# Kernel tuning notes

Measured on AMD Instinct MI355X. Metric: run time of the kernel, lower is better.

Reference implementation:

```python
import jax, jax.numpy as jnp
import numpy as np

B, S, D = 2, 2048, 1024
H = 16
K = 21  # tisa_num_kernels
HD = D // H


def setup_inputs() -> dict:
    key = jax.random.key(0)
    ks = jax.random.split(key, 7)
    x = jax.random.normal(ks[0], (B, S, D), dtype=jnp.float32)
    # in_proj: Linear(d_model, 3*d_model, bias=False); stored as (D, 3D) for x @ w
    w_in = jax.random.normal(ks[1], (D, 3 * D), dtype=jnp.float32) * (1.0 / np.sqrt(D))
    # gate: Linear(d_model, 2*d_model) with bias
    w_gate = jax.random.normal(ks[2], (D, 2 * D), dtype=jnp.float32) * (1.0 / np.sqrt(D))
    b_gate = jnp.zeros((2 * D,), dtype=jnp.float32)
    # TISA kernel params, one set of K kernels per head
    amplitudes = jax.random.normal(ks[3], (H, K), dtype=jnp.float32) * 0.1
    sharpness = jax.random.uniform(ks[4], (H, K), dtype=jnp.float32, minval=0.05, maxval=0.3)
    max_fv, min_fv = S // 2, 5
    offsets = jax.random.uniform(ks[5], (H, K), dtype=jnp.float32, minval=-float(max_fv), maxval=float(max_fv))
    return {"x": x, "w_in": w_in, "w_gate": w_gate, "b_gate": b_gate,
            "amplitudes": amplitudes, "sharpness": sharpness, "offsets": offsets}


def _tisa_bias(amplitudes, sharpness, offsets, seq_len):
    # Translation-invariant: score depends only on relative position j - i.
    # Compute scores over the 2S-1 unique relative positions, then gather.
    rel = jnp.arange(-(seq_len - 1), seq_len, dtype=jnp.float32)  # (2S-1,)
    # (H, K, 2S-1)
    d = rel[None, None, :] - offsets[:, :, None]
    scores = amplitudes[:, :, None] * jnp.exp(-jnp.abs(sharpness)[:, :, None] * d * d)
    scores = scores.sum(axis=1)  # (H, 2S-1)
    idx = jnp.arange(seq_len)
    rel_idx = idx[None, :] - idx[:, None] + (seq_len - 1)  # (S, S) in [0, 2S-2]
    return scores[:, rel_idx]  # (H, S, S)


def reference(x, w_in, w_gate, b_gate, amplitudes, sharpness, offsets):
    b, s, d = x.shape
    proj = x @ w_in  # (B, S, 3D); layout: [k | v | q]
    k, v, q = jnp.split(proj, 3, axis=-1)

    def heads(t):  # (B, S, D) -> (B, H, S, HD)
        return t.reshape(b, s, H, HD).transpose(0, 2, 1, 3)

    q, k, v = heads(q), heads(k), heads(v)
    scale = 1.0 / jnp.sqrt(jnp.float32(HD))
    scores = jnp.einsum('bhqd,bhkd->bhqk', q, k) * scale  # (B, H, S, S)
    scores = scores + _tisa_bias(amplitudes, sharpness, offsets, s)[None]
    weights = jax.nn.softmax(scores, axis=-1)
    attn = jnp.einsum('bhqk,bhkd->bhqd', weights, v)  # (B, H, S, HD)
    out = attn.transpose(0, 2, 1, 3).reshape(b, s, d)  # (B, S, D)
    gated = out @ w_gate + b_gate  # (B, S, 2D)
    a, g = jnp.split(gated, 2, axis=-1)
    return a * jax.nn.sigmoid(g)
```

## Files before the change

### kernel.cpp

```cpp
#include <hip/hip_runtime.h>
#include <math.h>

#define B_   2
#define S_   2048
#define D_   1024
#define H_   16
#define K_   21
#define HD_  64
#define D3_  3072
#define D2_  2048
#define REL_ 4095
#define LOG2E 1.44269504f

typedef __attribute__((ext_vector_type(8))) short bf16x8;
typedef __attribute__((ext_vector_type(8))) unsigned short u16x8;
typedef __attribute__((ext_vector_type(4))) float f32x4;

#define MFMA16(a, b, c) __builtin_amdgcn_mfma_f32_16x16x32_bf16((a), (b), (c), 0, 0, 0)

__device__ __forceinline__ unsigned short f2bf(float f) {
    union { float f; unsigned u; } v; v.f = f;
    return (unsigned short)((v.u + 0x7fffu + ((v.u >> 16) & 1u)) >> 16);
}
__device__ __forceinline__ float bf2f(unsigned short h) {
    union { unsigned u; float f; } v; v.u = ((unsigned)h) << 16;
    return v.f;
}
__device__ __forceinline__ float asf(unsigned u) {
    union { unsigned u; float f; } v; v.u = u; return v.f;
}
__device__ __forceinline__ float fexp2(float x) {
    float r;
    asm("v_exp_f32 %0, %1" : "=v"(r) : "v"(x));
    return r;
}
__device__ __forceinline__ unsigned cvtpk(float a, float b) {
    unsigned r;
    asm("v_cvt_pk_bf16_f32 %0, %1, %2" : "=v"(r) : "v"(a), "v"(b));
    return r;
}
#define SPLIT8(f, ph, pl)                                                      \
    {                                                                          \
        _Pragma("unroll")                                                      \
        for (int _t = 0; _t < 4; ++_t) ph.u[_t] = cvtpk(f[2*_t], f[2*_t+1]);   \
        _Pragma("unroll")                                                      \
        for (int _t = 0; _t < 4; ++_t) {                                       \
            float _h0 = asf(ph.u[_t] << 16);                                   \
            float _h1 = asf(ph.u[_t] & 0xffff0000u);                           \
            pl.u[_t] = cvtpk(f[2*_t] - _h0, f[2*_t+1] - _h1);                  \
        }                                                                      \
    }

__device__ __forceinline__ void gload16(const void* g, void* l) {
    __builtin_amdgcn_global_load_lds(
        (const __attribute__((address_space(1))) unsigned int*)g,
        (__attribute__((address_space(3))) unsigned int*)l, 16, 0, 0);
}

__global__ void tisa_bias_kernel(const float* __restrict__ amp,
                                 const float* __restrict__ shp,
                                 const float* __restrict__ off,
                                 float* __restrict__ bias_rel) {
    int idx = blockIdx.x * blockDim.x + threadIdx.x;
    if (idx >= H_ * REL_) return;
    int h = idx / REL_;
    int r = idx - h * REL_;
    float rel = (float)(r - (S_ - 1));
    float acc = 0.f;
    #pragma unroll
    for (int k = 0; k < K_; ++k) {
        float d = rel - off[h * K_ + k];
        acc = fmaf(amp[h * K_ + k], expf(-fabsf(shp[h * K_ + k]) * d * d), acc);
    }
    bias_rel[idx] = acc * LOG2E;
}

__global__ __launch_bounds__(256) void convert_x_kernel(
    const float* __restrict__ in, unsigned short* __restrict__ out)
{
    const int t   = blockIdx.x * 256 + threadIdx.x;
    const int row = t >> 7;
    const int c8  = (t & 127) * 8;
    const float* src = in + (size_t)row * D_ + c8;
    float v[8];
    *(float4*)&v[0] = *(const float4*)src;
    *(float4*)&v[4] = *(const float4*)(src + 4);
    unsigned short hi[8], lo[8];
    #pragma unroll
    for (int i = 0; i < 8; ++i) {
        hi[i] = f2bf(v[i]);
        lo[i] = f2bf(v[i] - bf2f(hi[i]));
    }
    const int kc = c8 >> 5;
    const int j0 = c8 & 31;
    unsigned short* op = out + (size_t)row * 2048 + kc * 64;
    *(u16x8*)&op[j0]      = *(u16x8*)&hi[0];
    *(u16x8*)&op[32 + j0] = *(u16x8*)&lo[0];
}

template<bool PERM>
__global__ __launch_bounds__(256) void convert_wT_kernel(
    const float* __restrict__ in, unsigned short* __restrict__ out, int Kd, int N)
{
    __shared__ float t[64][65];
    const int tid = threadIdx.x;
    const int k0 = blockIdx.y * 64;
    const int n0 = blockIdx.x * 64;
    {
        const int r  = tid >> 2;
        const int cq = (tid & 3) * 16;
        #pragma unroll
        for (int e = 0; e < 4; ++e) {
            float4 v = *(const float4*)&in[(size_t)(k0 + r) * N + n0 + cq + 4 * e];
            t[r][cq + 4 * e + 0] = v.x;
            t[r][cq + 4 * e + 1] = v.y;
            t[r][cq + 4 * e + 2] = v.z;
            t[r][cq + 4 * e + 3] = v.w;
        }
    }
    __syncthreads();
    {
        const int n  = tid >> 2;
        const int ks = (tid & 3) * 16;
        const int nkc = Kd >> 5;
        unsigned short hi[16], lo[16];
        #pragma unroll
        for (int i = 0; i < 16; ++i) {
            float v = t[ks + i][n];
            hi[i] = f2bf(v);
            lo[i] = f2bf(v - bf2f(hi[i]));
        }
        const int kg = k0 + ks;
        const int kc = kg >> 5;
        const int j0 = kg & 31;
        const int nsrc = n0 + n;
        const int dc = PERM ? ((nsrc < 1024) ? 2 * nsrc : 2 * (nsrc - 1024) + 1) : nsrc;
        unsigned short* op = out + (size_t)dc * (nkc * 64) + kc * 64;
        *(u16x8*)&op[j0]          = *(u16x8*)&hi[0];
        *(u16x8*)&op[j0 + 8]      = *(u16x8*)&hi[8];
        *(u16x8*)&op[32 + j0]     = *(u16x8*)&lo[0];
        *(u16x8*)&op[32 + j0 + 8] = *(u16x8*)&lo[8];
    }
}

template<int EPI>
__global__ __launch_bounds__(256) void gemm_split_kernel(
    const void* Ap, const unsigned short* __restrict__ Bt,
    const float* __restrict__ bias, float* C,
    int N, int Kd, int lda, int ldc)
{
    __shared__ unsigned short Al[2][128 * 64];
    __shared__ unsigned short Bl[2][128 * 64];
    const int tid  = threadIdx.x;
    const int w    = tid >> 6;
    const int lane = tid & 63;
    const int c    = lane & 15;
    const int g    = lane >> 4;
    const int m0   = blockIdx.y * 128;
    const int n0   = blockIdx.x * 128;
    const int wrow = (w >> 1) * 64;
    const int wcol = (w & 1) * 64;
    const int nkc  = Kd >> 5;

    f32x4 acc[4][4];
    #pragma unroll
    for (int i = 0; i < 4; ++i)
        #pragma unroll
        for (int j = 0; j < 4; ++j) acc[i][j] = (f32x4){0.f, 0.f, 0.f, 0.f};

    const int srowB  = w * 8 + (lane >> 3);
    const int sslotB = lane & 7;

#define STAGE_AB(buf, kcv)                                                    \
    {                                                                         \
        _Pragma("unroll")                                                     \
        for (int i = 0; i < 4; ++i) {                                         \
            const int row = w * 32 + i * 8 + (lane >> 3);                     \
            const char* src = (const char*)Ap + (size_t)(m0 + row) * lda      \
                            + (kcv) * 128 + (((lane & 7) ^ (row & 7)) << 4);  \
            gload16(src, (char*)Al[buf] + w * 4096 + i * 1024);               \
        }                                                                     \
        _Pragma("unroll")                                                     \
        for (int i = 0; i < 4; ++i) {                                         \
            const int n = i * 32 + srowB;                                     \
            const unsigned short* src = Bt                                    \
                + ((size_t)(n0 + n) * nkc + (kcv)) * 64                       \
                + ((sslotB ^ (n & 7)) << 3);                                  \
            gload16(src, (char*)Bl[buf] + i * 4096 + w * 1024);               \
        }                                                                     \
    }

    STAGE_AB(0, 0);
    int cur = 0;

    for (int kc = 0; kc < nkc; ++kc) {
        if (kc + 1 < nkc) {
            STAGE_AB(cur ^ 1, kc + 1);
            asm volatile("s_waitcnt vmcnt(8)" ::: "memory");
        } else {
            asm volatile("s_waitcnt vmcnt(0)" ::: "memory");
        }
        __builtin_amdgcn_s_barrier();
        __builtin_amdgcn_sched_barrier(0);

        bf16x8 ah[4], al[4], bh[4], bl[4];
        #pragma unroll
        for (int f = 0; f < 4; ++f) {
            const int m = wrow + f * 16 + c;
            const char* rp = (const char*)Al[cur] + m * 128;
            ah[f] = *(const bf16x8*)(rp + (((g + 0) ^ (m & 7)) << 4));
            al[f] = *(const bf16x8*)(rp + (((g + 4) ^ (m & 7)) << 4));
            const int n = wcol + f * 16 + c;
            const char* rq = (const char*)Bl[cur] + n * 128;
            bh[f] = *(const bf16x8*)(rq + (((g + 0) ^ (n & 7)) << 4));
            bl[f] = *(const bf16x8*)(rq + (((g + 4) ^ (n & 7)) << 4));
        }
        #pragma unroll
        for (int mf = 0; mf < 4; ++mf)
            #pragma unroll
            for (int nf = 0; nf < 4; ++nf) {
                acc[mf][nf] = MFMA16(ah[mf], bh[nf], acc[mf][nf]);
                acc[mf][nf] = MFMA16(al[mf], bh[nf], acc[mf][nf]);
                acc[mf][nf] = MFMA16(ah[mf], bl[nf], acc[mf][nf]);
            }
        asm volatile("s_waitcnt lgkmcnt(0)" ::: "memory");
        __builtin_amdgcn_s_barrier();
        cur ^= 1;
    }
#undef STAGE_AB

    if (EPI == 1) {
        if (n0 < 1024) {
            #pragma unroll
            for (int mf = 0; mf < 4; ++mf)
                #pragma unroll
                for (int r = 0; r < 4; ++r) {
                    const int row = m0 + wrow + mf * 16 + g * 4 + r;
                    char* rowB = (char*)C + (size_t)row * 12288;
                    #pragma unroll
                    for (int nf = 0; nf < 4; ++nf) {
                        const int col = n0 + wcol + nf * 16 + c;
                        const float val = acc[mf][nf][r];
                        const unsigned short hi = f2bf(val);
                        *(unsigned short*)(rowB + 4096 + 2 * col) = hi;
                        *(unsigned short*)(rowB + 6144 + 2 * col) = f2bf(val - bf2f(hi));
                    }
                }
        } else if (n0 < 2048) {
            #pragma unroll
            for (int mf = 0; mf < 4; ++mf) {
                const int row0 = m0 + wrow + mf * 16 + g * 4;
                const int s2 = (row0 & 2047) * 2;
                const size_t ibase = (size_t)(row0 >> 11) * 1024;
                #pragma unroll
                for (int nf = 0; nf < 4; ++nf) {
                    const int d = n0 - 1024 + wcol + nf * 16 + c;
                    ushort4 hv, lv;
                    {
                        float v0 = acc[mf][nf][0], v1 = acc[mf][nf][1];
                        float v2 = acc[mf][nf][2], v3 = acc[mf][nf][3];
                        hv.x = f2bf(v0); lv.x = f2bf(v0 - bf2f(hv.x));
                        hv.y = f2bf(v1); lv.y = f2bf(v1 - bf2f(hv.y));
                        hv.z = f2bf(v2); lv.z = f2bf(v2 - bf2f(hv.z));
                        hv.w = f2bf(v3); lv.w = f2bf(v3 - bf2f(hv.w));
                    }
                    char* base = (char*)C + (ibase + d) * (size_t)24576 + s2;
                    *(ushort4*)base           = hv;
                    *(ushort4*)(base + 12288) = lv;
                }
            }
        } else {
            #pragma unroll
            for (int mf = 0; mf < 4; ++mf)
                #pragma unroll
                for (int r = 0; r < 4; ++r) {
                    const int row = m0 + wrow + mf * 16 + g * 4 + r;
                    float* cp = &C[(size_t)row * ldc + n0 + wcol + c];
                    #pragma unroll
                    for (int nf = 0; nf < 4; ++nf)
                        cp[nf * 16] = acc[mf][nf][r];
                }
        }
    } else {
        float bgs[4];
        #pragma unroll
        for (int nf = 0; nf < 4; ++nf) {
            const int jc = n0 + wcol + nf * 16 + c;
            bgs[nf] = bias[(jc & 1) ? (1024 + (jc >> 1)) : (jc >> 1)];
        }
        #pragma unroll
        for (int mf = 0; mf < 4; ++mf)
            #pragma unroll
            for (int r = 0; r < 4; ++r) {
                const int row = m0 + wrow + mf * 16 + g * 4 + r;
                #pragma unroll
                for (int nf = 0; nf < 4; ++nf) {
                    const int jc = n0 + wcol + nf * 16 + c;
                    const float val = acc[mf][nf][r] + bgs[nf];
                    const float part = __shfl_xor(val, 1);
                    if (!(c & 1))
                        C[(size_t)row * ldc + (jc >> 1)] = val / (1.f + __expf(-part));
                }
            }
    }
}

__global__ __launch_bounds__(512) void attn_mfma_kernel(
    const float* projf, char* projB, const float* __restrict__ bias_rel)
{
    __shared__ unsigned short KHI[4096], KLO[4096], VHI[4096], VLO[4096];
    __shared__ unsigned short PHI[4096], PLO[4096];
    __shared__ float bias_s[192];

    const int tid  = threadIdx.x;
    const int w    = tid >> 6;
    const int lane = tid & 63;
    const int c    = lane & 15;
    const int g    = lane >> 4;
    const int bid  = blockIdx.x;
    const int xcd  = bid & 7;
    const int slot = bid >> 3;
    const int qt   = slot & 15;
    const int p    = (slot >> 4) * 8 + xcd;
    const int h    = p >> 1;
    const int b    = p & 1;
    const int qbase = qt * 128;
    const size_t rowbase = (size_t)b * S_;
    const int q    = 16 * w + c;
    const int psw  = (q & 3) ^ ((q >> 2) & 1);

    bf16x8 Qhi[2], Qlo[2];
    {
        const float* qp = projf + (rowbase + qbase + q) * D3_ + 2 * D_ + h * HD_;
        #pragma unroll
        for (int ck = 0; ck < 2; ++ck) {
            float q8[8];
            *(float4*)&q8[0] = *(const float4*)(qp + ck * 32 + g * 8);
            *(float4*)&q8[4] = *(const float4*)(qp + ck * 32 + g * 8 + 4);
            union { unsigned u[4]; bf16x8 v; } ph, pl;
            const float* f = q8;
            SPLIT8(f, ph, pl);
            Qhi[ck] = ph.v;
            Qlo[ck] = pl.v;
        }
    }

    f32x4 o_acc[4];
    #pragma unroll
    for (int n = 0; n < 4; ++n) o_acc[n] = (f32x4){0.f, 0.f, 0.f, 0.f};
    float m_run = -INFINITY;
    float l_run = 0.f;

    const int srow = tid >> 3;
    const int gsl  = (tid & 7) ^ (srow & 7);
    uint4 rkh, rkl, rvh, rvl;
    float breg = 0.f;

#define LOADKV(ktv)                                                            \
    {                                                                          \
        const int kbase_ = (ktv) * 64;                                         \
        const char* ks = projB + (rowbase + kbase_ + srow) * (size_t)12288     \
                       + 4096 + h * 128 + gsl * 16;                            \
        rkh = *(const uint4*)ks;  rkl = *(const uint4*)(ks + 2048);            \
        const char* vs = projB + (size_t)(b * 1024 + h * HD_ + srow) * 24576   \
                       + (size_t)kbase_ * 2 + gsl * 16;                        \
        rvh = *(const uint4*)vs;  rvl = *(const uint4*)(vs + 12288);           \
        if (tid < 191)                                                         \
            breg = bias_rel[h * REL_ + kbase_ - qbase + 1920 + tid];           \
    }

    LOADKV(0);

    for (int kt = 0; kt < S_ / 64; ++kt) {
        __syncthreads();
        {
            const int d = srow * 128 + (tid & 7) * 16;
            *(uint4*)((char*)KHI + d) = rkh;
            *(uint4*)((char*)KLO + d) = rkl;
            *(uint4*)((char*)VHI + d) = rvh;
            *(uint4*)((char*)VLO + d) = rvl;
            if (tid < 191) bias_s[tid] = breg;
        }
        if (kt + 1 < S_ / 64) LOADKV(kt + 1);
        __syncthreads();

        f32x4 sf[4];
        __builtin_amdgcn_s_setprio(1);
        #pragma unroll
        for (int f = 0; f < 4; ++f) {
            f32x4 acc = (f32x4){0.f, 0.f, 0.f, 0.f};
            const int krow = f * 16 + c;
            const unsigned short* kbp = KHI + krow * 64;
            const unsigned short* klp = KLO + krow * 64;
            #pragma unroll
            for (int ck = 0; ck < 2; ++ck) {
                const int s = ((ck * 4 + g) ^ (krow & 7)) * 8;
                bf16x8 kh  = *(const bf16x8*)(kbp + s);
                bf16x8 kl8 = *(const bf16x8*)(klp + s);
                acc = MFMA16(kh, Qhi[ck], acc);
                acc = MFMA16(kl8, Qhi[ck], acc);
                acc = MFMA16(kh, Qlo[ck], acc);
            }
            sf[f] = acc;
        }
        __builtin_amdgcn_s_setprio(0);

        #pragma unroll
        for (int f = 0; f < 4; ++f) {
            const int tb = 16 * f + 4 * g - q + 127;
            #pragma unroll
            for (int r = 0; r < 4; ++r)
                sf[f][r] = fmaf(sf[f][r], 0.125f * LOG2E, bias_s[tb + r]);
        }

        float pm[4];
        #pragma unroll
        for (int f = 0; f < 4; ++f)
            pm[f] = fmaxf(fmaxf(sf[f][0], sf[f][1]), fmaxf(sf[f][2], sf[f][3]));
        float mt = fmaxf(fmaxf(pm[0], pm[1]), fmaxf(pm[2], pm[3]));
        mt = fmaxf(mt, __shfl_xor(mt, 16));
        mt = fmaxf(mt, __shfl_xor(mt, 32));
        if (!__all(mt <= m_run + 11.5415603f)) {
            const float mn = fmaxf(m_run, mt);
            const float sc = fexp2(m_run - mn);
            l_run *= sc;
            m_run = mn;
            #pragma unroll
            for (int r = 0; r < 4; ++r) {
                const float scr = __shfl(sc, 20 * g + r);
                #pragma unroll
                for (int n = 0; n < 4; ++n) o_acc[n][r] *= scr;
            }
        }
        float ps[4];
        #pragma unroll
        for (int f = 0; f < 4; ++f) {
            #pragma unroll
            for (int r = 0; r < 4; ++r)
                sf[f][r] = fexp2(sf[f][r] - m_run);
            ps[f] = (sf[f][0] + sf[f][1]) + (sf[f][2] + sf[f][3]);
        }
        float rs = (ps[0] + ps[1]) + (ps[2] + ps[3]);
        rs += __shfl_xor(rs, 16);
        rs += __shfl_xor(rs, 32);
        l_run += rs;

        #pragma unroll
        for (int ck = 0; ck < 2; ++ck) {
            #pragma unroll
            for (int f2 = 0; f2 < 2; ++f2) {
                const int f = 2 * ck + f2;
                const unsigned uh0 = cvtpk(sf[f][0], sf[f][1]);
                const unsigned uh1 = cvtpk(sf[f][2], sf[f][3]);
                const float r0 = sf[f][0] - asf(uh0 << 16);
                const float r1 = sf[f][1] - asf(uh0 & 0xffff0000u);
                const float r2 = sf[f][2] - asf(uh1 << 16);
                const float r3 = sf[f][3] - asf(uh1 & 0xffff0000u);
                const unsigned ul0 = cvtpk(r0, r1);
                const unsigned ul1 = cvtpk(r2, r3);
                const int byte = q * 64
                    + ((((2 * f2 + (g >> 1)) ^ psw) << 4) + ((g & 1) << 3));
                uint2 vh2; vh2.x = uh0; vh2.y = uh1;
                uint2 vl2; vl2.x = ul0; vl2.y = ul1;
                *(uint2*)((char*)PHI + byte) = vh2;
                *(uint2*)((char*)PLO + byte) = vl2;
            }
            asm volatile("s_waitcnt lgkmcnt(0)" ::: "memory");
            const int rbyte = q * 64 + ((g ^ psw) << 4);
            bf16x8 pah = *(const bf16x8*)((char*)PHI + rbyte);
            bf16x8 pal = *(const bf16x8*)((char*)PLO + rbyte);
            __builtin_amdgcn_s_setprio(1);
            #pragma unroll
            for (int n = 0; n < 4; ++n) {
                const int d = 16 * n + c;
                const int s = ((ck * 4 + g) ^ (d & 7)) * 8;
                bf16x8 vh = *(const bf16x8*)(VHI + d * 64 + s);
                bf16x8 vl = *(const bf16x8*)(VLO + d * 64 + s);
                o_acc[n] = MFMA16(pah, vh, o_acc[n]);
                o_acc[n] = MFMA16(pal, vh, o_acc[n]);
                o_acc[n] = MFMA16(pah, vl, o_acc[n]);
            }
            __builtin_amdgcn_s_setprio(0);
        }
    }
#undef LOADKV

    const float inv = 1.f / l_run;
    #pragma unroll
    for (int r = 0; r < 4; ++r) {
        const float invr = __shfl(inv, 20 * g + r);
        unsigned short* op = (unsigned short*)(projB
            + (rowbase + qbase + 16 * w + 4 * g + r) * (size_t)12288 + 8192);
        #pragma unroll
        for (int n = 0; n < 4; ++n) {
            const float v = o_acc[n][r] * invr;
            const int col = h * HD_ + 16 * n + c;
            const int kc2 = col >> 5;
            const int j   = col & 31;
            const unsigned short hi = f2bf(v);
            op[kc2 * 64 + j]      = hi;
            op[kc2 * 64 + 32 + j] = f2bf(v - bf2f(hi));
        }
    }
}

extern "C" void kernel_launch(void* const* d_in, const int* in_sizes, int n_in,
                              void* d_out, int out_size, void* d_ws, size_t ws_size,
                              hipStream_t stream) {
    const float* x      = (const float*)d_in[0];
    const float* w_in   = (const float*)d_in[1];
    const float* w_gate = (const float*)d_in[2];
    const float* b_gate = (const float*)d_in[3];
    const float* amp    = (const float*)d_in[4];
    const float* shp    = (const float*)d_in[5];
    const float* off    = (const float*)d_in[6];
    float* outp = (float*)d_out;

    char* ws = (char*)d_ws;
    float*    proj     = (float*)ws;
    float*    bias_rel = (float*)(ws + 50331648);
    unsigned short* wT = (unsigned short*)(ws + 50331648 + 262144);
    unsigned short* xc = (unsigned short*)d_out;

    tisa_bias_kernel<<<(H_ * REL_ + 255) / 256, 256, 0, stream>>>(amp, shp, off, bias_rel);
    convert_x_kernel<<<2048, 256, 0, stream>>>(x, xc);
    convert_wT_kernel<false><<<dim3(D3_ / 64, D_ / 64), 256, 0, stream>>>(w_in, wT, D_, D3_);
    gemm_split_kernel<1><<<dim3(D3_ / 128, 32), 256, 0, stream>>>(
        xc, wT, nullptr, proj, D3_, D_, 4096, D3_);
    convert_wT_kernel<true><<<dim3(D2_ / 64, D_ / 64), 256, 0, stream>>>(w_gate, wT, D_, D2_);
    attn_mfma_kernel<<<512, 512, 0, stream>>>(proj, ws, bias_rel);
    gemm_split_kernel<2><<<dim3(D2_ / 128, 32), 256, 0, stream>>>(
        ws + 8192, wT, b_gate, outp, D2_, D_, 12288, D_);
}
```

Before: 272.2 us.

## Give each attention wave two query subtiles and load K/V directly into LDS

The attention kernel now runs 4 waves of 256 threads, each handling 32 queries as two 16-row subtiles. Each K and V fragment read from LDS feeds two MFMAs, so LDS traffic per MFMA is halved and MFMA issue is denser. The K/V tile staging switches from register prefetch of the next tile to direct global-to-LDS loads issued after the barrier. That removes the register staging but also the overlap of the next tile's load with compute. Fewer waves per block and more accumulator registers per wave reduce the ability to hide latency.

```diff
diff --git a/kernel.cpp b/kernel.cpp
--- a/kernel.cpp
+++ b/kernel.cpp
@@ -305,7 +305,7 @@
     }
 }
 
-__global__ __launch_bounds__(512) void attn_mfma_kernel(
+__global__ __launch_bounds__(256) void attn_mfma_kernel(
     const float* projf, char* projB, const float* __restrict__ bias_rel)
 {
     __shared__ unsigned short KHI[4096], KLO[4096], VHI[4096], VLO[4096];
@@ -326,12 +326,12 @@
     const int b    = p & 1;
     const int qbase = qt * 128;
     const size_t rowbase = (size_t)b * S_;
-    const int q    = 16 * w + c;
-    const int psw  = (q & 3) ^ ((q >> 2) & 1);
-
-    bf16x8 Qhi[2], Qlo[2];
-    {
-        const float* qp = projf + (rowbase + qbase + q) * D3_ + 2 * D_ + h * HD_;
+
+    bf16x8 Qhi[2][2], Qlo[2][2];
+    #pragma unroll
+    for (int qs = 0; qs < 2; ++qs) {
+        const float* qp = projf + (rowbase + qbase + 32 * w + 16 * qs + c) * D3_
+                        + 2 * D_ + h * HD_;
         #pragma unroll
         for (int ck = 0; ck < 2; ++ck) {
             float q8[8];
@@ -340,55 +340,51 @@
             union { unsigned u[4]; bf16x8 v; } ph, pl;
             const float* f = q8;
             SPLIT8(f, ph, pl);
-            Qhi[ck] = ph.v;
-            Qlo[ck] = pl.v;
-        }
-    }
-
-    f32x4 o_acc[4];
+            Qhi[qs][ck] = ph.v;
+            Qlo[qs][ck] = pl.v;
+        }
+    }
+
+    f32x4 o_acc[2][4];
     #pragma unroll
-    for (int n = 0; n < 4; ++n) o_acc[n] = (f32x4){0.f, 0.f, 0.f, 0.f};
-    float m_run = -INFINITY;
-    float l_run = 0.f;
-
-    const int srow = tid >> 3;
-    const int gsl  = (tid & 7) ^ (srow & 7);
-    uint4 rkh, rkl, rvh, rvl;
+    for (int qs = 0; qs < 2; ++qs)
+        #pragma unroll
+        for (int n = 0; n < 4; ++n) o_acc[qs][n] = (f32x4){0.f, 0.f, 0.f, 0.f};
+    float m_run[2] = {-INFINITY, -INFINITY};
+    float l_run[2] = {0.f, 0.f};
+
+    const int gsl = (lane & 7) ^ (lane >> 3);
     float breg = 0.f;
-
-#define LOADKV(ktv)                                                            \
-    {                                                                          \
-        const int kbase_ = (ktv) * 64;                                         \
-        const char* ks = projB + (rowbase + kbase_ + srow) * (size_t)12288     \
-                       + 4096 + h * 128 + gsl * 16;                            \
-        rkh = *(const uint4*)ks;  rkl = *(const uint4*)(ks + 2048);            \
-        const char* vs = projB + (size_t)(b * 1024 + h * HD_ + srow) * 24576   \
-                       + (size_t)kbase_ * 2 + gsl * 16;                        \
-        rvh = *(const uint4*)vs;  rvl = *(const uint4*)(vs + 12288);           \
-        if (tid < 191)                                                         \
-            breg = bias_rel[h * REL_ + kbase_ - qbase + 1920 + tid];           \
-    }
-
-    LOADKV(0);
+    if (tid < 191) breg = bias_rel[h * REL_ - qbase + 1920 + tid];
 
     for (int kt = 0; kt < S_ / 64; ++kt) {
+        const int kbase = kt * 64;
         __syncthreads();
-        {
-            const int d = srow * 128 + (tid & 7) * 16;
-            *(uint4*)((char*)KHI + d) = rkh;
-            *(uint4*)((char*)KLO + d) = rkl;
-            *(uint4*)((char*)VHI + d) = rvh;
-            *(uint4*)((char*)VLO + d) = rvl;
-            if (tid < 191) bias_s[tid] = breg;
-        }
-        if (kt + 1 < S_ / 64) LOADKV(kt + 1);
+        #pragma unroll
+        for (int i = 0; i < 2; ++i) {
+            const int row = 16 * w + i * 8 + (lane >> 3);
+            const char* ks = projB + (rowbase + kbase + row) * (size_t)12288
+                           + 4096 + h * 128 + gsl * 16;
+            gload16(ks,        (char*)KHI + w * 2048 + i * 1024);
+            gload16(ks + 2048, (char*)KLO + w * 2048 + i * 1024);
+            const char* vs = projB + (size_t)(b * 1024 + h * HD_ + row) * 24576
+                           + (size_t)kbase * 2 + gsl * 16;
+            gload16(vs,         (char*)VHI + w * 2048 + i * 1024);
+            gload16(vs + 12288, (char*)VLO + w * 2048 + i * 1024);
+        }
+        if (tid < 191) {
+            bias_s[tid] = breg;
+            if (kt + 1 < S_ / 64)
+                breg = bias_rel[h * REL_ + (kt + 1) * 64 - qbase + 1920 + tid];
+        }
         __syncthreads();
 
-        f32x4 sf[4];
+        f32x4 sf[2][4];
         __builtin_amdgcn_s_setprio(1);
         #pragma unroll
         for (int f = 0; f < 4; ++f) {
-            f32x4 acc = (f32x4){0.f, 0.f, 0.f, 0.f};
+            f32x4 a0 = (f32x4){0.f, 0.f, 0.f, 0.f};
+            f32x4 a1 = (f32x4){0.f, 0.f, 0.f, 0.f};
             const int krow = f * 16 + c;
             const unsigned short* kbp = KHI + krow * 64;
             const unsigned short* klp = KLO + krow * 64;
@@ -397,78 +393,97 @@
                 const int s = ((ck * 4 + g) ^ (krow & 7)) * 8;
                 bf16x8 kh  = *(const bf16x8*)(kbp + s);
                 bf16x8 kl8 = *(const bf16x8*)(klp + s);
-                acc = MFMA16(kh, Qhi[ck], acc);
-                acc = MFMA16(kl8, Qhi[ck], acc);
-                acc = MFMA16(kh, Qlo[ck], acc);
-            }
-            sf[f] = acc;
+                a0 = MFMA16(kh, Qhi[0][ck], a0);
+                a1 = MFMA16(kh, Qhi[1][ck], a1);
+                a0 = MFMA16(kl8, Qhi[0][ck], a0);
+                a1 = MFMA16(kl8, Qhi[1][ck], a1);
+                a0 = MFMA16(kh, Qlo[0][ck], a0);
+                a1 = MFMA16(kh, Qlo[1][ck], a1);
+            }
+            sf[0][f] = a0;
+            sf[1][f] = a1;
         }
         __builtin_amdgcn_s_setprio(0);
 
         #pragma unroll
-        for (int f = 0; f < 4; ++f) {
-            const int tb = 16 * f + 4 * g - q + 127;
-            #pragma unroll
-            for (int r = 0; r < 4; ++r)
-                sf[f][r] = fmaf(sf[f][r], 0.125f * LOG2E, bias_s[tb + r]);
-        }
-
-        float pm[4];
-        #pragma unroll
-        for (int f = 0; f < 4; ++f)
-            pm[f] = fmaxf(fmaxf(sf[f][0], sf[f][1]), fmaxf(sf[f][2], sf[f][3]));
-        float mt = fmaxf(fmaxf(pm[0], pm[1]), fmaxf(pm[2], pm[3]));
-        mt = fmaxf(mt, __shfl_xor(mt, 16));
-        mt = fmaxf(mt, __shfl_xor(mt, 32));
-        if (!__all(mt <= m_run + 11.5415603f)) {
-            const float mn = fmaxf(m_run, mt);
-            const float sc = fexp2(m_run - mn);
-            l_run *= sc;
-            m_run = mn;
-            #pragma unroll
-            for (int r = 0; r < 4; ++r) {
-                const float scr = __shfl(sc, 20 * g + r);
-                #pragma unroll
-                for (int n = 0; n < 4; ++n) o_acc[n][r] *= scr;
-            }
-        }
-        float ps[4];
-        #pragma unroll
-        for (int f = 0; f < 4; ++f) {
-            #pragma unroll
-            for (int r = 0; r < 4; ++r)
-                sf[f][r] = fexp2(sf[f][r] - m_run);
-            ps[f] = (sf[f][0] + sf[f][1]) + (sf[f][2] + sf[f][3]);
-        }
-        float rs = (ps[0] + ps[1]) + (ps[2] + ps[3]);
-        rs += __shfl_xor(rs, 16);
-        rs += __shfl_xor(rs, 32);
-        l_run += rs;
+        for (int qs = 0; qs < 2; ++qs) {
+            const int qe = 32 * w + 16 * qs + c;
+            #pragma unroll
+            for (int f = 0; f < 4; ++f) {
+                const int tb = 16 * f + 4 * g - qe + 127;
+                #pragma unroll
+                for (int r = 0; r < 4; ++r)
+                    sf[qs][f][r] = fmaf(sf[qs][f][r], 0.125f * LOG2E, bias_s[tb + r]);
+            }
+            float pm[4];
+            #pragma unroll
+            for (int f = 0; f < 4; ++f)
+                pm[f] = fmaxf(fmaxf(sf[qs][f][0], sf[qs][f][1]),
+                              fmaxf(sf[qs][f][2], sf[qs][f][3]));
+            float mt = fmaxf(fmaxf(pm[0], pm[1]), fmaxf(pm[2], pm[3]));
+            mt = fmaxf(mt, __shfl_xor(mt, 16));
+            mt = fmaxf(mt, __shfl_xor(mt, 32));
+            if (!__all(mt <= m_run[qs] + 11.5415603f)) {
+                const float mn = fmaxf(m_run[qs], mt);
+                const float sc = fexp2(m_run[qs] - mn);
+                l_run[qs] *= sc;
+                m_run[qs] = mn;
+                #pragma unroll
+                for (int r = 0; r < 4; ++r) {
+                    const float scr = __shfl(sc, 20 * g + r);
+                    #pragma unroll
+                    for (int n = 0; n < 4; ++n) o_acc[qs][n][r] *= scr;
+                }
+            }
+            float ps[4];
+            #pragma unroll
+            for (int f = 0; f < 4; ++f) {
+                #pragma unroll
+                for (int r = 0; r < 4; ++r)
+                    sf[qs][f][r] = fexp2(sf[qs][f][r] - m_run[qs]);
+                ps[f] = (sf[qs][f][0] + sf[qs][f][1]) + (sf[qs][f][2] + sf[qs][f][3]);
+            }
+            float rs = (ps[0] + ps[1]) + (ps[2] + ps[3]);
+            rs += __shfl_xor(rs, 16);
+            rs += __shfl_xor(rs, 32);
+            l_run[qs] += rs;
+        }
 
         #pragma unroll
         for (int ck = 0; ck < 2; ++ck) {
             #pragma unroll
-            for (int f2 = 0; f2 < 2; ++f2) {
-                const int f = 2 * ck + f2;
-                const unsigned uh0 = cvtpk(sf[f][0], sf[f][1]);
-                const unsigned uh1 = cvtpk(sf[f][2], sf[f][3]);
-                const float r0 = sf[f][0] - asf(uh0 << 16);
-                const float r1 = sf[f][1] - asf(uh0 & 0xffff0000u);
-                const float r2 = sf[f][2] - asf(uh1 << 16);
-                const float r3 = sf[f][3] - asf(uh1 & 0xffff0000u);
-                const unsigned ul0 = cvtpk(r0, r1);
-                const unsigned ul1 = cvtpk(r2, r3);
-                const int byte = q * 64
-                    + ((((2 * f2 + (g >> 1)) ^ psw) << 4) + ((g & 1) << 3));
-                uint2 vh2; vh2.x = uh0; vh2.y = uh1;
-                uint2 vl2; vl2.x = ul0; vl2.y = ul1;
-                *(uint2*)((char*)PHI + byte) = vh2;
-                *(uint2*)((char*)PLO + byte) = vl2;
+            for (int qs = 0; qs < 2; ++qs) {
+                const int qe  = 32 * w + 16 * qs + c;
+                const int psw = (qe & 3) ^ ((qe >> 2) & 1);
+                #pragma unroll
+                for (int f2 = 0; f2 < 2; ++f2) {
+                    const int f = 2 * ck + f2;
+                    const unsigned uh0 = cvtpk(sf[qs][f][0], sf[qs][f][1]);
+                    const unsigned uh1 = cvtpk(sf[qs][f][2], sf[qs][f][3]);
+                    const float r0 = sf[qs][f][0] - asf(uh0 << 16);
+                    const float r1 = sf[qs][f][1] - asf(uh0 & 0xffff0000u);
+                    const float r2 = sf[qs][f][2] - asf(uh1 << 16);
+                    const float r3 = sf[qs][f][3] - asf(uh1 & 0xffff0000u);
+                    const unsigned ul0 = cvtpk(r0, r1);
+                    const unsigned ul1 = cvtpk(r2, r3);
+                    const int byte = qe * 64
+                        + ((((2 * f2 + (g >> 1)) ^ psw) << 4) + ((g & 1) << 3));
+                    uint2 vh2; vh2.x = uh0; vh2.y = uh1;
+                    uint2 vl2; vl2.x = ul0; vl2.y = ul1;
+                    *(uint2*)((char*)PHI + byte) = vh2;
+                    *(uint2*)((char*)PLO + byte) = vl2;
+                }
             }
             asm volatile("s_waitcnt lgkmcnt(0)" ::: "memory");
-            const int rbyte = q * 64 + ((g ^ psw) << 4);
-            bf16x8 pah = *(const bf16x8*)((char*)PHI + rbyte);
-            bf16x8 pal = *(const bf16x8*)((char*)PLO + rbyte);
+            bf16x8 pah[2], pal[2];
+            #pragma unroll
+            for (int qs = 0; qs < 2; ++qs) {
+                const int qe  = 32 * w + 16 * qs + c;
+                const int psw = (qe & 3) ^ ((qe >> 2) & 1);
+                const int rbyte = qe * 64 + ((g ^ psw) << 4);
+                pah[qs] = *(const bf16x8*)((char*)PHI + rbyte);
+                pal[qs] = *(const bf16x8*)((char*)PLO + rbyte);
+            }
             __builtin_amdgcn_s_setprio(1);
             #pragma unroll
             for (int n = 0; n < 4; ++n) {
@@ -476,30 +491,36 @@
                 const int s = ((ck * 4 + g) ^ (d & 7)) * 8;
                 bf16x8 vh = *(const bf16x8*)(VHI + d * 64 + s);
                 bf16x8 vl = *(const bf16x8*)(VLO + d * 64 + s);
-                o_acc[n] = MFMA16(pah, vh, o_acc[n]);
-                o_acc[n] = MFMA16(pal, vh, o_acc[n]);
-                o_acc[n] = MFMA16(pah, vl, o_acc[n]);
+                o_acc[0][n] = MFMA16(pah[0], vh, o_acc[0][n]);
+                o_acc[1][n] = MFMA16(pah[1], vh, o_acc[1][n]);
+                o_acc[0][n] = MFMA16(pal[0], vh, o_acc[0][n]);
+                o_acc[1][n] = MFMA16(pal[1], vh, o_acc[1][n]);
+                o_acc[0][n] = MFMA16(pah[0], vl, o_acc[0][n]);
+                o_acc[1][n] = MFMA16(pah[1], vl, o_acc[1][n]);
             }
             __builtin_amdgcn_s_setprio(0);
         }
     }
-#undef LOADKV
-
-    const float inv = 1.f / l_run;
+
     #pragma unroll
-    for (int r = 0; r < 4; ++r) {
-        const float invr = __shfl(inv, 20 * g + r);
-        unsigned short* op = (unsigned short*)(projB
-            + (rowbase + qbase + 16 * w + 4 * g + r) * (size_t)12288 + 8192);
-        #pragma unroll
-        for (int n = 0; n < 4; ++n) {
-            const float v = o_acc[n][r] * invr;
-            const int col = h * HD_ + 16 * n + c;
-            const int kc2 = col >> 5;
-            const int j   = col & 31;
-            const unsigned short hi = f2bf(v);
-            op[kc2 * 64 + j]      = hi;
-            op[kc2 * 64 + 32 + j] = f2bf(v - bf2f(hi));
+    for (int qs = 0; qs < 2; ++qs) {
+        const float inv = 1.f / l_run[qs];
+        #pragma unroll
+        for (int r = 0; r < 4; ++r) {
+            const float invr = __shfl(inv, 20 * g + r);
+            unsigned short* op = (unsigned short*)(projB
+                + (rowbase + qbase + 32 * w + 16 * qs + 4 * g + r) * (size_t)12288
+                + 8192);
+            #pragma unroll
+            for (int n = 0; n < 4; ++n) {
+                const float v = o_acc[qs][n][r] * invr;
+                const int col = h * HD_ + 16 * n + c;
+                const int kc2 = col >> 5;
+                const int j   = col & 31;
+                const unsigned short hi = f2bf(v);
+                op[kc2 * 64 + j]      = hi;
+                op[kc2 * 64 + 32 + j] = f2bf(v - bf2f(hi));
+            }
         }
     }
 }
@@ -528,7 +549,7 @@
     gemm_split_kernel<1><<<dim3(D3_ / 128, 32), 256, 0, stream>>>(
         xc, wT, nullptr, proj, D3_, D_, 4096, D3_);
     convert_wT_kernel<true><<<dim3(D2_ / 64, D_ / 64), 256, 0, stream>>>(w_gate, wT, D_, D2_);
-    attn_mfma_kernel<<<512, 512, 0, stream>>>(proj, ws, bias_rel);
+    attn_mfma_kernel<<<512, 256, 0, stream>>>(proj, ws, bias_rel);
     gemm_split_kernel<2><<<dim3(D2_ / 128, 32), 256, 0, stream>>>(
         ws + 8192, wT, b_gate, outp, D2_, D_, 12288, D_);
 }
```

New measurement: 283.1 us. 1.04x slower.
